# Performance work log

Measured on AMD Instinct MI355X. Metric: run time of the kernel, lower is better.

Reference implementation:

```python
import jax, jax.numpy as jnp
import numpy as np


def _highway(x, Ws, bs):
    # Ws: [n_hw, 2H, H] (torch Linear layout), bs: [n_hw, 2H]
    H = x.shape[-1]
    for i in range(Ws.shape[0]):
        proj = jnp.einsum('bsh,oh->bso', x, Ws[i]) + bs[i]
        nonlin = jax.nn.relu(proj[..., :H])
        gate = jax.nn.sigmoid(proj[..., H:])
        x = gate * x + (1.0 - gate) * nonlin
    return x


def setup_inputs() -> dict:
    key = jax.random.key(0)
    ks = jax.random.split(key, 10)
    B, S, H, L, W, NHW = 32, 512, 512, 2, 4, 2
    scale = 1.0 / np.sqrt(H)
    return {
        'inputs': jax.random.normal(ks[0], (B, S, H), dtype=jnp.float32),
        'masks': jnp.ones((B, S), dtype=jnp.int32),
        'fwd_pads': jax.random.normal(ks[1], (L, W, H), dtype=jnp.float32) * scale,
        'bwd_pads': jax.random.normal(ks[2], (L, W, H), dtype=jnp.float32) * scale,
        'fwd_ws': jax.random.normal(ks[3], (L, W + 1), dtype=jnp.float32),
        'bwd_ws': jax.random.normal(ks[4], (L, W + 1), dtype=jnp.float32),
        'fwd_hw_W': jax.random.normal(ks[5], (L, NHW, 2 * H, H), dtype=jnp.float32) * scale,
        'fwd_hw_b': jax.random.normal(ks[6], (L, NHW, 2 * H), dtype=jnp.float32) * 0.1,
        'bwd_hw_W': jax.random.normal(ks[7], (L, NHW, 2 * H, H), dtype=jnp.float32) * scale,
        'bwd_hw_b': jax.random.normal(ks[8], (L, NHW, 2 * H), dtype=jnp.float32) * 0.1,
    }


def reference(inputs, masks, fwd_pads, bwd_pads, fwd_ws, bwd_ws,
              fwd_hw_W, fwd_hw_b, bwd_hw_W, bwd_hw_b):
    # inputs: [B,S,H]; masks unused (as in the torch module)
    B, S, H = inputs.shape
    L, W, _ = fwd_pads.shape
    fwd_in = inputs
    bwd_in = inputs
    outs = []
    for l in range(L):
        fp = jnp.broadcast_to(fwd_pads[l], (B, W, H))
        bp = jnp.broadcast_to(bwd_pads[l], (B, W, H))
        pf = jnp.concatenate([fp, fwd_in, bp], axis=1)  # [B, S+2W, H]
        pb = jnp.concatenate([fp, bwd_in, bp], axis=1)
        # forward window at t covers padded positions t..t+W (causal)
        f_win = jnp.stack([pf[:, k:k + S] for k in range(W + 1)], axis=0)  # [W+1,B,S,H]
        f_out = jnp.einsum('k,kbsh->bsh', fwd_ws[l], f_win)
        # backward window at t covers padded positions t+W..t+2W (anti-causal)
        b_win = jnp.stack([pb[:, W + k:W + k + S] for k in range(W + 1)], axis=0)
        b_out = jnp.einsum('k,kbsh->bsh', bwd_ws[l], b_win)
        f_out = _highway(f_out, fwd_hw_W[l], fwd_hw_b[l])
        b_out = _highway(b_out, bwd_hw_W[l], bwd_hw_b[l])
        fwd_in, bwd_in = f_out, b_out
        outs.append(jnp.concatenate([f_out, b_out], axis=-1))
    return jnp.stack(outs, axis=0)  # [L, B, S, 2H]
```

## Files before the change

kernel.cpp:

```cpp
#include <hip/hip_runtime.h>
#include <hip/hip_bf16.h>

typedef __attribute__((ext_vector_type(8))) short bf16x8;
typedef __attribute__((ext_vector_type(4))) float floatx4;

#define B_ 32
#define S_ 512
#define H_ 512
#define M_ (B_*S_)
#define K_ 512
#define N_ 1024

__device__ __forceinline__ void gload_lds16(const void* g, void* l) {
  __builtin_amdgcn_global_load_lds(
      (const __attribute__((address_space(1))) void*)g,
      (__attribute__((address_space(3))) void*)l, 16, 0, 0);
}

__global__ void cvt2_kernel(const float* __restrict__ s0, const float* __restrict__ s1,
                            __hip_bfloat16* __restrict__ d0, __hip_bfloat16* __restrict__ d1) {
  int t = blockIdx.x * 256 + threadIdx.x;
  const float* src;
  __hip_bfloat16* dst;
  int i;
  if (t < 524288) { src = s0; dst = d0; i = t; }
  else            { src = s1; dst = d1; i = t - 524288; }
  float4 v = *(const float4*)(src + (size_t)i * 4);
  union { ushort4 u; __hip_bfloat16 h[4]; } pk;
  pk.h[0] = __float2bfloat16(v.x);
  pk.h[1] = __float2bfloat16(v.y);
  pk.h[2] = __float2bfloat16(v.z);
  pk.h[3] = __float2bfloat16(v.w);
  *(ushort4*)((unsigned short*)dst + (size_t)i * 4) = pk.u;
}

__global__ void conv_kernel(const float* __restrict__ inf, const float* __restrict__ inb,
                            int instride,
                            const float* __restrict__ fpad, const float* __restrict__ bpad,
                            const float* __restrict__ fw, const float* __restrict__ bw,
                            __hip_bfloat16* __restrict__ xaf, __hip_bfloat16* __restrict__ xab) {
  int t = blockIdx.x * 256 + threadIdx.x;
  int dir = blockIdx.y;
  int row = t >> 7;
  int hv  = (t & 127) << 2;
  int s = row & (S_ - 1);
  float4 a = make_float4(0.f, 0.f, 0.f, 0.f);
  if (dir == 0) {
#pragma unroll
    for (int k = 0; k < 5; ++k) {
      float w = fw[k];
      const float* src = (s + k < 4) ? (fpad + (size_t)(s + k) * H_ + hv)
                                     : (inf + (size_t)(row + k - 4) * instride + hv);
      float4 v = *(const float4*)src;
      a.x += w * v.x; a.y += w * v.y; a.z += w * v.z; a.w += w * v.w;
    }
  } else {
#pragma unroll
    for (int k = 0; k < 5; ++k) {
      float w = bw[k];
      const float* src = (s + k < S_) ? (inb + (size_t)(row + k) * instride + hv)
                                      : (bpad + (size_t)(s + k - S_) * H_ + hv);
      float4 v = *(const float4*)src;
      a.x += w * v.x; a.y += w * v.y; a.z += w * v.z; a.w += w * v.w;
    }
  }
  __hip_bfloat16* xa = dir ? xab : xaf;
  union { ushort4 u; __hip_bfloat16 h[4]; } pk;
  pk.h[0] = __float2bfloat16(a.x);
  pk.h[1] = __float2bfloat16(a.y);
  pk.h[2] = __float2bfloat16(a.z);
  pk.h[3] = __float2bfloat16(a.w);
  *(ushort4*)((unsigned short*)xa + (size_t)row * H_ + hv) = pk.u;
}

__global__ __launch_bounds__(512, 2)
void hw_gemm(const __hip_bfloat16* __restrict__ Af, const __hip_bfloat16* __restrict__ Ab,
             const __hip_bfloat16* __restrict__ Wf, const __hip_bfloat16* __restrict__ Wb,
             const float* __restrict__ biasf, const float* __restrict__ biasb,
             __hip_bfloat16* __restrict__ Anf, __hip_bfloat16* __restrict__ Anb,
             float* __restrict__ outp, int final_mode) {
  __shared__ __align__(16) char smem[65536];

  const int tid = threadIdx.x;
  const int lane = tid & 63, wave = tid >> 6;
  const int wm = wave >> 1, wn = wave & 1;
  const int quad = lane >> 4, l16 = lane & 15;
  const int dir = blockIdx.z;

  const int n = blockIdx.x;
  const int by = n & 63, bx = n >> 6;
  const int m0 = by * 256;
  const int h0 = bx * 128;

  const __hip_bfloat16* A = dir ? Ab : Af;
  const __hip_bfloat16* Wm = dir ? Wb : Wf;
  const float* bias = dir ? biasb : biasf;
  __hip_bfloat16* An = dir ? Anb : Anf;

  floatx4 acc[4][8];
#pragma unroll
  for (int i = 0; i < 4; ++i)
#pragma unroll
    for (int j = 0; j < 8; ++j) acc[i][j] = (floatx4){0.f, 0.f, 0.f, 0.f};

  const int srow = lane >> 2;
  const int skk  = (((lane & 3) ^ ((lane >> 3) & 3)) << 3);
  const int key  = (l16 >> 1) & 3;
  const int xkp0 = bx * 4 + wn * 2;
  const int xkp1 = xkp0 + 1;

  const __hip_bfloat16* aptr[2];
  const __hip_bfloat16* bptr[2];
#pragma unroll
  for (int c = 0; c < 2; ++c) {
    const int chunk = wave * 2 + c;
    aptr[c] = A + (size_t)(m0 + chunk * 16 + srow) * K_ + skk;
    const int brow = chunk * 16 + srow;
    const int wnp = brow >> 7, rr = brow & 127;
    const int wrow = (rr < 64) ? (h0 + wnp * 64 + rr)
                               : (512 + h0 + wnp * 64 + (rr - 64));
    bptr[c] = Wm + (size_t)wrow * K_ + skk;
  }

#pragma unroll
  for (int c = 0; c < 2; ++c) {
    const int chunk = wave * 2 + c;
    gload_lds16(aptr[c], smem + chunk * 1024);
    gload_lds16(bptr[c], smem + 16384 + chunk * 1024);
  }
#pragma unroll
  for (int c = 0; c < 2; ++c) {
    const int chunk = wave * 2 + c;
    gload_lds16(aptr[c] + 32, smem + 32768 + chunk * 1024);
    gload_lds16(bptr[c] + 32, smem + 32768 + 16384 + chunk * 1024);
  }

  unsigned int xsp[4][4][2];
  int cur = 0;
  for (int kp = 0; kp < 16; ++kp) {
    const __hip_bfloat16* cA = (const __hip_bfloat16*)(smem + (cur << 15));
    const __hip_bfloat16* cB = (const __hip_bfloat16*)(smem + (cur << 15) + 16384);

    if (kp < 15) asm volatile("s_waitcnt vmcnt(4)" ::: "memory");
    else         asm volatile("s_waitcnt vmcnt(0)" ::: "memory");
    __builtin_amdgcn_s_barrier();

    if (kp == xkp0) {
      const unsigned short* pA = (const unsigned short*)cA;
#pragma unroll
      for (int i = 0; i < 4; ++i)
#pragma unroll
        for (int jj = 0; jj < 2; ++jj)
#pragma unroll
          for (int rh = 0; rh < 2; ++rh) {
            const int ra0 = wm * 64 + i * 16 + quad * 4 + rh * 2;
            const int ra1 = ra0 + 1;
            const int c2 = jj * 16 + l16;
            unsigned int lo = pA[ra0 * 32 + ((((c2 >> 3) ^ ((ra0 >> 1) & 3)) << 3) | (c2 & 7))];
            unsigned int hi = pA[ra1 * 32 + ((((c2 >> 3) ^ ((ra1 >> 1) & 3)) << 3) | (c2 & 7))];
            xsp[i][jj][rh] = lo | (hi << 16);
          }
    }
    if (kp == xkp1) {
      const unsigned short* pA = (const unsigned short*)cA;
#pragma unroll
      for (int i = 0; i < 4; ++i)
#pragma unroll
        for (int jj = 0; jj < 2; ++jj)
#pragma unroll
          for (int rh = 0; rh < 2; ++rh) {
            const int ra0 = wm * 64 + i * 16 + quad * 4 + rh * 2;
            const int ra1 = ra0 + 1;
            const int c2 = jj * 16 + l16;
            unsigned int lo = pA[ra0 * 32 + ((((c2 >> 3) ^ ((ra0 >> 1) & 3)) << 3) | (c2 & 7))];
            unsigned int hi = pA[ra1 * 32 + ((((c2 >> 3) ^ ((ra1 >> 1) & 3)) << 3) | (c2 & 7))];
            xsp[i][2 + jj][rh] = lo | (hi << 16);
          }
    }

    __builtin_amdgcn_s_setprio(1);
    bf16x8 av[4];
#pragma unroll
    for (int i = 0; i < 4; ++i) {
      const int ra = wm * 64 + i * 16 + l16;
      av[i] = *(const bf16x8*)&cA[ra * 32 + ((quad ^ key) << 3)];
    }
#pragma unroll
    for (int jh = 0; jh < 2; ++jh) {
      bf16x8 bv[4];
#pragma unroll
      for (int jj = 0; jj < 4; ++jj) {
        const int rb = wn * 128 + (jh * 4 + jj) * 16 + l16;
        bv[jj] = *(const bf16x8*)&cB[rb * 32 + ((quad ^ key) << 3)];
      }
#pragma unroll
      for (int i = 0; i < 4; ++i)
#pragma unroll
        for (int jj = 0; jj < 4; ++jj)
          acc[i][jh * 4 + jj] =
              __builtin_amdgcn_mfma_f32_16x16x32_bf16(av[i], bv[jj], acc[i][jh * 4 + jj], 0, 0, 0);
    }
    __builtin_amdgcn_s_setprio(0);

    asm volatile("s_waitcnt lgkmcnt(0)" ::: "memory");
    __builtin_amdgcn_s_barrier();

    if (kp < 14) {
      char* nb = smem + (cur << 15);
      const int kb = (kp + 2) * 32;
#pragma unroll
      for (int c = 0; c < 2; ++c) {
        const int chunk = wave * 2 + c;
        gload_lds16(aptr[c] + kb, nb + chunk * 1024);
        gload_lds16(bptr[c] + kb, nb + 16384 + chunk * 1024);
      }
    }
    cur ^= 1;
  }

  float bnl[4], bgt[4];
#pragma unroll
  for (int j = 0; j < 4; ++j) {
    const int c = h0 + wn * 64 + j * 16 + l16;
    bnl[j] = bias[c];
    bgt[j] = bias[512 + c];
  }

  if (final_mode) {
    float* ft = (float*)smem;
#pragma unroll
    for (int p = 0; p < 2; ++p) {
      if (wn == p) {
#pragma unroll
        for (int i = 0; i < 4; ++i)
#pragma unroll
          for (int r = 0; r < 4; ++r) {
            const int rl = wm * 64 + i * 16 + quad * 4 + r;
#pragma unroll
            for (int j = 0; j < 4; ++j) {
              float pn = acc[i][j][r] + bnl[j];
              float pg = acc[i][j + 4][r] + bgt[j];
              float g = 1.f / (1.f + __expf(-pg));
              unsigned int u = xsp[i][j][r >> 1];
              unsigned int bits = (r & 1) ? (u >> 16) : (u & 0xffffu);
              float xo = __uint_as_float(bits << 16);
              ft[rl * 64 + j * 16 + l16] = g * xo + (1.f - g) * fmaxf(pn, 0.f);
            }
          }
      }
      __syncthreads();
#pragma unroll
      for (int q = 0; q < 8; ++q) {
        const int rl = q * 32 + (tid >> 4);
        const int cc = (tid & 15) * 4;
        float4 v = *(const float4*)&ft[rl * 64 + cc];
        *(float4*)&outp[(size_t)(m0 + rl) * N_ + dir * H_ + h0 + p * 64 + cc] = v;
      }
      __syncthreads();
    }
  } else {
    __hip_bfloat16* bt = (__hip_bfloat16*)smem;
#pragma unroll
    for (int i = 0; i < 4; ++i)
#pragma unroll
      for (int r = 0; r < 4; ++r) {
        const int rl = wm * 64 + i * 16 + quad * 4 + r;
#pragma unroll
        for (int j = 0; j < 4; ++j) {
          float pn = acc[i][j][r] + bnl[j];
          float pg = acc[i][j + 4][r] + bgt[j];
          float g = 1.f / (1.f + __expf(-pg));
          unsigned int u = xsp[i][j][r >> 1];
          unsigned int bits = (r & 1) ? (u >> 16) : (u & 0xffffu);
          float xo = __uint_as_float(bits << 16);
          bt[rl * 128 + wn * 64 + j * 16 + l16] =
              __float2bfloat16(g * xo + (1.f - g) * fmaxf(pn, 0.f));
        }
      }
    __syncthreads();
    const unsigned short* src = (const unsigned short*)smem;
#pragma unroll
    for (int p = 0; p < 8; ++p) {
      const int rl = p * 32 + (tid >> 4);
      const int cc = (tid & 15) * 8;
      int4 v = *(const int4*)(src + rl * 128 + cc);
      *(int4*)((unsigned short*)An + (size_t)(m0 + rl) * H_ + h0 + cc) = v;
    }
  }
}

extern "C" void kernel_launch(void* const* d_in, const int* in_sizes, int n_in,
                              void* d_out, int out_size, void* d_ws, size_t ws_size,
                              hipStream_t stream) {
  const float* inputs   = (const float*)d_in[0];
  const float* fwd_pads = (const float*)d_in[2];
  const float* bwd_pads = (const float*)d_in[3];
  const float* fwd_ws_p = (const float*)d_in[4];
  const float* bwd_ws_p = (const float*)d_in[5];
  const float* fwd_hw_W = (const float*)d_in[6];
  const float* fwd_hw_b = (const float*)d_in[7];
  const float* bwd_hw_W = (const float*)d_in[8];
  const float* bwd_hw_b = (const float*)d_in[9];
  float* out = (float*)d_out;

  char* ws = (char*)d_ws;
  size_t off = 0;
  __hip_bfloat16* Wbf = (__hip_bfloat16*)(ws + off); off += (size_t)4194304 * 2;
  __hip_bfloat16* xa0f = (__hip_bfloat16*)(ws + off); off += (size_t)M_ * H_ * 2;
  __hip_bfloat16* xa0b = (__hip_bfloat16*)(ws + off); off += (size_t)M_ * H_ * 2;
  __hip_bfloat16* xa1f = (__hip_bfloat16*)(ws + off); off += (size_t)M_ * H_ * 2;
  __hip_bfloat16* xa1b = (__hip_bfloat16*)(ws + off); off += (size_t)M_ * H_ * 2;

  cvt2_kernel<<<4096, 256, 0, stream>>>(fwd_hw_W, bwd_hw_W, Wbf, Wbf + (size_t)2097152);

  for (int l = 0; l < 2; ++l) {
    const float *inf, *inb;
    int instride;
    if (l == 0) { inf = inputs; inb = inputs; instride = H_; }
    else        { inf = out;    inb = out + H_; instride = N_; }
    conv_kernel<<<dim3(8192, 2), 256, 0, stream>>>(
        inf, inb, instride,
        fwd_pads + (size_t)l * 4 * H_, bwd_pads + (size_t)l * 4 * H_,
        fwd_ws_p + l * 5, bwd_ws_p + l * 5,
        xa0f, xa0b);

    hw_gemm<<<dim3(256, 1, 2), 512, 0, stream>>>(
        xa0f, xa0b,
        Wbf + (size_t)(l * 2) * 524288, Wbf + (size_t)2097152 + (size_t)(l * 2) * 524288,
        fwd_hw_b + (l * 2) * 1024, bwd_hw_b + (l * 2) * 1024,
        xa1f, xa1b, nullptr, 0);

    hw_gemm<<<dim3(256, 1, 2), 512, 0, stream>>>(
        xa1f, xa1b,
        Wbf + (size_t)(l * 2 + 1) * 524288, Wbf + (size_t)2097152 + (size_t)(l * 2 + 1) * 524288,
        fwd_hw_b + (l * 2 + 1) * 1024, bwd_hw_b + (l * 2 + 1) * 1024,
        nullptr, nullptr, out + (size_t)l * M_ * N_, 1);
  }
}
```

Before: 428.1 us.

## Deepen highway GEMM pipeline to four LDS stages with split-phase loads

New measurement: 448.7 us. 4.8% more time.

```diff
diff --git a/kernel.cpp b/kernel.cpp
--- a/kernel.cpp
+++ b/kernel.cpp
@@ -79,7 +79,7 @@
              const float* __restrict__ biasf, const float* __restrict__ biasb,
              __hip_bfloat16* __restrict__ Anf, __hip_bfloat16* __restrict__ Anb,
              float* __restrict__ outp, int final_mode) {
-  __shared__ __align__(16) char smem[65536];
+  extern __shared__ __align__(16) char smem[];
 
   const int tid = threadIdx.x;
   const int lane = tid & 63, wave = tid >> 6;
@@ -123,28 +123,34 @@
   }
 
 #pragma unroll
-  for (int c = 0; c < 2; ++c) {
-    const int chunk = wave * 2 + c;
-    gload_lds16(aptr[c], smem + chunk * 1024);
-    gload_lds16(bptr[c], smem + 16384 + chunk * 1024);
-  }
-#pragma unroll
-  for (int c = 0; c < 2; ++c) {
-    const int chunk = wave * 2 + c;
-    gload_lds16(aptr[c] + 32, smem + 32768 + chunk * 1024);
-    gload_lds16(bptr[c] + 32, smem + 32768 + 16384 + chunk * 1024);
-  }
+  for (int tt = 0; tt < 3; ++tt)
+#pragma unroll
+    for (int c = 0; c < 2; ++c) {
+      const int chunk = wave * 2 + c;
+      gload_lds16(aptr[c] + tt * 32, smem + (tt << 15) + chunk * 1024);
+      gload_lds16(bptr[c] + tt * 32, smem + (tt << 15) + 16384 + chunk * 1024);
+    }
+  asm volatile("s_waitcnt vmcnt(8)" ::: "memory");
+  __builtin_amdgcn_s_barrier();
 
   unsigned int xsp[4][4][2];
-  int cur = 0;
   for (int kp = 0; kp < 16; ++kp) {
-    const __hip_bfloat16* cA = (const __hip_bfloat16*)(smem + (cur << 15));
-    const __hip_bfloat16* cB = (const __hip_bfloat16*)(smem + (cur << 15) + 16384);
-
-    if (kp < 15) asm volatile("s_waitcnt vmcnt(4)" ::: "memory");
-    else         asm volatile("s_waitcnt vmcnt(0)" ::: "memory");
-    __builtin_amdgcn_s_barrier();
-
+    const __hip_bfloat16* cA = (const __hip_bfloat16*)(smem + ((kp & 3) << 15));
+    const __hip_bfloat16* cB = (const __hip_bfloat16*)(smem + ((kp & 3) << 15) + 16384);
+    char* nb = smem + (((kp + 3) & 3) << 15);
+    const int kb = (kp + 3) * 32;
+
+    bf16x8 av[4], bv[4];
+#pragma unroll
+    for (int i = 0; i < 4; ++i) {
+      const int ra = wm * 64 + i * 16 + l16;
+      av[i] = *(const bf16x8*)&cA[ra * 32 + ((quad ^ key) << 3)];
+    }
+#pragma unroll
+    for (int jj = 0; jj < 4; ++jj) {
+      const int rb = wn * 128 + jj * 16 + l16;
+      bv[jj] = *(const bf16x8*)&cB[rb * 32 + ((quad ^ key) << 3)];
+    }
     if (kp == xkp0) {
       const unsigned short* pA = (const unsigned short*)cA;
 #pragma unroll
@@ -177,45 +183,46 @@
             xsp[i][2 + jj][rh] = lo | (hi << 16);
           }
     }
-
+    if (kp < 13) {
+#pragma unroll
+      for (int c = 0; c < 2; ++c)
+        gload_lds16(aptr[c] + kb, nb + (wave * 2 + c) * 1024);
+    }
+    asm volatile("" ::: "memory");
+    __builtin_amdgcn_s_barrier();
     __builtin_amdgcn_s_setprio(1);
-    bf16x8 av[4];
-#pragma unroll
-    for (int i = 0; i < 4; ++i) {
-      const int ra = wm * 64 + i * 16 + l16;
-      av[i] = *(const bf16x8*)&cA[ra * 32 + ((quad ^ key) << 3)];
-    }
-#pragma unroll
-    for (int jh = 0; jh < 2; ++jh) {
-      bf16x8 bv[4];
-#pragma unroll
-      for (int jj = 0; jj < 4; ++jj) {
-        const int rb = wn * 128 + (jh * 4 + jj) * 16 + l16;
-        bv[jj] = *(const bf16x8*)&cB[rb * 32 + ((quad ^ key) << 3)];
-      }
-#pragma unroll
-      for (int i = 0; i < 4; ++i)
-#pragma unroll
-        for (int jj = 0; jj < 4; ++jj)
-          acc[i][jh * 4 + jj] =
-              __builtin_amdgcn_mfma_f32_16x16x32_bf16(av[i], bv[jj], acc[i][jh * 4 + jj], 0, 0, 0);
-    }
+#pragma unroll
+    for (int i = 0; i < 4; ++i)
+#pragma unroll
+      for (int jj = 0; jj < 4; ++jj)
+        acc[i][jj] = __builtin_amdgcn_mfma_f32_16x16x32_bf16(av[i], bv[jj], acc[i][jj], 0, 0, 0);
     __builtin_amdgcn_s_setprio(0);
-
-    asm volatile("s_waitcnt lgkmcnt(0)" ::: "memory");
+    asm volatile("" ::: "memory");
     __builtin_amdgcn_s_barrier();
 
-    if (kp < 14) {
-      char* nb = smem + (cur << 15);
-      const int kb = (kp + 2) * 32;
-#pragma unroll
-      for (int c = 0; c < 2; ++c) {
-        const int chunk = wave * 2 + c;
-        gload_lds16(aptr[c] + kb, nb + chunk * 1024);
-        gload_lds16(bptr[c] + kb, nb + 16384 + chunk * 1024);
-      }
-    }
-    cur ^= 1;
+#pragma unroll
+    for (int jj = 0; jj < 4; ++jj) {
+      const int rb = wn * 128 + (4 + jj) * 16 + l16;
+      bv[jj] = *(const bf16x8*)&cB[rb * 32 + ((quad ^ key) << 3)];
+    }
+    if (kp < 13) {
+#pragma unroll
+      for (int c = 0; c < 2; ++c)
+        gload_lds16(bptr[c] + kb, nb + 16384 + (wave * 2 + c) * 1024);
+    }
+    asm volatile("" ::: "memory");
+    __builtin_amdgcn_s_barrier();
+    __builtin_amdgcn_s_setprio(1);
+#pragma unroll
+    for (int i = 0; i < 4; ++i)
+#pragma unroll
+      for (int jj = 0; jj < 4; ++jj)
+        acc[i][4 + jj] = __builtin_amdgcn_mfma_f32_16x16x32_bf16(av[i], bv[jj], acc[i][4 + jj], 0, 0, 0);
+    __builtin_amdgcn_s_setprio(0);
+    if (kp < 13)       asm volatile("s_waitcnt vmcnt(8)" ::: "memory");
+    else if (kp == 13) asm volatile("s_waitcnt vmcnt(4)" ::: "memory");
+    else if (kp == 14) asm volatile("s_waitcnt vmcnt(0)" ::: "memory");
+    __builtin_amdgcn_s_barrier();
   }
 
   float bnl[4], bgt[4];
@@ -303,6 +310,13 @@
   const float* bwd_hw_b = (const float*)d_in[9];
   float* out = (float*)d_out;
 
+  static int attr_done = 0;
+  if (!attr_done) {
+    (void)hipFuncSetAttribute((const void*)hw_gemm,
+                              hipFuncAttributeMaxDynamicSharedMemorySize, 131072);
+    attr_done = 1;
+  }
+
   char* ws = (char*)d_ws;
   size_t off = 0;
   __hip_bfloat16* Wbf = (__hip_bfloat16*)(ws + off); off += (size_t)4194304 * 2;
@@ -324,13 +338,13 @@
         fwd_ws_p + l * 5, bwd_ws_p + l * 5,
         xa0f, xa0b);
 
-    hw_gemm<<<dim3(256, 1, 2), 512, 0, stream>>>(
+    hw_gemm<<<dim3(256, 1, 2), 512, 131072, stream>>>(
         xa0f, xa0b,
         Wbf + (size_t)(l * 2) * 524288, Wbf + (size_t)2097152 + (size_t)(l * 2) * 524288,
         fwd_hw_b + (l * 2) * 1024, bwd_hw_b + (l * 2) * 1024,
         xa1f, xa1b, nullptr, 0);
 
-    hw_gemm<<<dim3(256, 1, 2), 512, 0, stream>>>(
+    hw_gemm<<<dim3(256, 1, 2), 512, 131072, stream>>>(
         xa1f, xa1b,
         Wbf + (size_t)(l * 2 + 1) * 524288, Wbf + (size_t)2097152 + (size_t)(l * 2 + 1) * 524288,
         fwd_hw_b + (l * 2 + 1) * 1024, bwd_hw_b + (l * 2 + 1) * 1024,
```
